# Performance work log

Hardware: AMD Instinct MI355X
Metric: run time of the kernel (lower is better)

Reference implementation:

```python
import jax, jax.numpy as jnp
import numpy as np

B, T, I, L, D, O = 256, 512, 512, 128, 4, 2
LN_EPS = 1e-5

def setup_inputs() -> dict:
    key = jax.random.key(0)
    ks = jax.random.split(key, 7)
    x = jax.random.normal(ks[0], (B, T, I), jnp.float32)
    # Xavier-ish scaling keeps the recurrence numerically tame
    W_in = jax.random.normal(ks[1], (L, D, I), jnp.float32) * (1.0 / np.sqrt(I))
    W_liquid = jax.random.normal(ks[2], (L, D, L), jnp.float32) * (1.0 / np.sqrt(L))
    W_gate = jax.random.normal(ks[3], (L, D), jnp.float32)
    b_liquid = jnp.zeros((L,), jnp.float32)
    W_out = jax.random.normal(ks[4], (O, L), jnp.float32) * (1.0 / np.sqrt(L))
    b_out = jnp.zeros((O,), jnp.float32)
    ln_w = jnp.ones((L,), jnp.float32)
    ln_b = jnp.zeros((L,), jnp.float32)
    leaky_rate = jnp.asarray(0.3, jnp.float32)
    return {"x": x, "W_in": W_in, "W_liquid": W_liquid, "W_gate": W_gate,
            "b_liquid": b_liquid, "W_out": W_out, "b_out": b_out,
            "ln_w": ln_w, "ln_b": ln_b, "leaky_rate": leaky_rate}

def reference(x, W_in, W_liquid, W_gate, b_liquid, W_out, b_out, ln_w, ln_b, leaky_rate):
    # Liquid dendritic RNN. Dropout is identity (eval mode).
    gate = jax.nn.sigmoid(W_gate)                                   # [L,D]
    # Input branch has no recurrent dependency -> batch it over all timesteps
    in_br = jax.nn.relu(jnp.einsum('ldi,bti->btld', W_in, x))       # [B,T,L,D]
    merged_in = jnp.einsum('btld,ld->btl', in_br, gate)             # [B,T,L]
    alpha = jax.nn.sigmoid(leaky_rate)

    def step(state, m_in_t):                                        # state [B,L]
        rec_br = jax.nn.relu(jnp.einsum('ldh,bh->bld', W_liquid, state))
        merged_rec = jnp.einsum('bld,ld->bl', rec_br, gate)
        li = m_in_t + merged_rec + b_liquid                         # [B,L]
        mu = jnp.mean(li, axis=-1, keepdims=True)
        var = jnp.var(li, axis=-1, keepdims=True)
        li = (li - mu) * jax.lax.rsqrt(var + LN_EPS) * ln_w + ln_b
        new_state = (1.0 - alpha) * state + alpha * jnp.tanh(li)
        return new_state, None

    state0 = jnp.zeros((x.shape[0], W_in.shape[0]), x.dtype)
    final_state, _ = jax.lax.scan(step, state0, jnp.swapaxes(merged_in, 0, 1))
    return final_state @ W_out.T + b_out                            # [B,O]
```

## Files before the change

### kernel.cpp

```cpp
#include <hip/hip_runtime.h>
#include <hip/hip_bf16.h>
#include <stdint.h>


typedef __bf16 bf16x8 __attribute__((ext_vector_type(8)));
typedef float f32x4_t __attribute__((ext_vector_type(4)));

__device__ inline unsigned short f2bf(float f) {
    union { float f; unsigned u; } v; v.f = f;
    unsigned r = v.u + 0x7fffu + ((v.u >> 16) & 1u);
    return (unsigned short)(r >> 16);
}

__device__ inline unsigned cvt_pk_bf16(float lo, float hi) {
    unsigned r;
    asm("v_cvt_pk_bf16_f32 %0, %1, %2" : "=v"(r) : "v"(lo), "v"(hi));
    return r;
}

__device__ inline void lds_barrier() {
    asm volatile("s_waitcnt lgkmcnt(0)" ::: "memory");
    __builtin_amdgcn_s_barrier();
}

__device__ inline float bfly16_add(float x) {
    float a, b;
    asm volatile("v_mov_b32 %0, %2\n\t"
                 "v_mov_b32 %1, %2\n\t"
                 "v_permlane16_swap_b32 %0, %1"
                 : "=&v"(a), "=&v"(b) : "v"(x));
    return a + b;
}
__device__ inline float bfly32_add(float x) {
    float a, b;
    asm volatile("v_mov_b32 %0, %2\n\t"
                 "v_mov_b32 %1, %2\n\t"
                 "v_permlane32_swap_b32 %0, %1"
                 : "=&v"(a), "=&v"(b) : "v"(x));
    return a + b;
}

__global__ __launch_bounds__(256, 2)
void gemm_in_kernel(const float* __restrict__ x, const float* __restrict__ W_in,
                    const float* __restrict__ W_gate, const float* __restrict__ b_liq,
                    float* __restrict__ mt)
{
    __shared__ unsigned short As[128 * 32];
    __shared__ unsigned short Bs[128 * 32];

    const int tid = threadIdx.x;
    const int wid  = blockIdx.x;
    const int xcd  = wid & 7;
    const int slot = wid >> 3;
    const int n0 = (slot & 3) * 128;
    const int m0 = ((slot >> 2) + xcd * 128) * 128;

    const int lane = tid & 63;
    const int widw = tid >> 6;
    const int wr = widw >> 1, wc = widw & 1;
    const int fr = lane & 15, fq = lane >> 4;

    f32x4_t acc[4][4];
    #pragma unroll
    for (int i = 0; i < 4; ++i)
        #pragma unroll
        for (int j = 0; j < 4; ++j)
            acc[i][j] = (f32x4_t){0.f, 0.f, 0.f, 0.f};

    for (int k0 = 0; k0 < 512; k0 += 32) {
        #pragma unroll
        for (int p = 0; p < 4; ++p) {
            int ch = tid + p * 256;
            int r  = ch >> 3;
            int c  = ch & 7;
            float4 va = *(const float4*)(x    + (size_t)(m0 + r) * 512 + k0 + c * 4);
            float4 vb = *(const float4*)(W_in + (size_t)(n0 + r) * 512 + k0 + c * 4);
            uint2 ua, ub;
            ua.x = cvt_pk_bf16(va.x, va.y);
            ua.y = cvt_pk_bf16(va.z, va.w);
            ub.x = cvt_pk_bf16(vb.x, vb.y);
            ub.y = cvt_pk_bf16(vb.z, vb.w);
            *(uint2*)(&As[r * 32 + c * 4]) = ua;
            *(uint2*)(&Bs[r * 32 + c * 4]) = ub;
        }
        __syncthreads();

        bf16x8 af[4], bfr[4];
        #pragma unroll
        for (int mi = 0; mi < 4; ++mi)
            af[mi] = *(const bf16x8*)(&As[(wr * 64 + mi * 16 + fr) * 32 + fq * 8]);
        #pragma unroll
        for (int ni = 0; ni < 4; ++ni)
            bfr[ni] = *(const bf16x8*)(&Bs[(wc * 64 + ni * 16 + fr) * 32 + fq * 8]);

        #pragma unroll
        for (int mi = 0; mi < 4; ++mi)
            #pragma unroll
            for (int ni = 0; ni < 4; ++ni)
                acc[mi][ni] = __builtin_amdgcn_mfma_f32_16x16x32_bf16(
                                  af[mi], bfr[ni], acc[mi][ni], 0, 0, 0);
        __syncthreads();
    }

    float gv[4], blq[4];
    #pragma unroll
    for (int ni = 0; ni < 4; ++ni) {
        int n = n0 + wc * 64 + ni * 16 + fr;
        gv[ni]  = 1.f / (1.f + __expf(-W_gate[n]));
        blq[ni] = b_liq[n >> 2];
    }
    #pragma unroll
    for (int mi = 0; mi < 4; ++mi) {
        #pragma unroll
        for (int ni = 0; ni < 4; ++ni) {
            int n = n0 + wc * 64 + ni * 16 + fr;
            int l = n >> 2;
            #pragma unroll
            for (int j = 0; j < 4; ++j) {
                float v = acc[mi][ni][j];
                float r = fmaxf(v, 0.f) * gv[ni];
                r += __shfl_xor(r, 1);
                r += __shfl_xor(r, 2);
                if ((lane & 3) == 0) {
                    int row = m0 + wr * 64 + mi * 16 + fq * 4 + j;
                    int bb = row >> 9;
                    int tt = row & 511;
                    mt[(size_t)bb * 65536 + (size_t)l * 512 + tt] = r + blq[ni];
                }
            }
        }
    }
}

__global__ __launch_bounds__(256, 1)
void scan_kernel(const float* __restrict__ mt, const float* __restrict__ W_liq,
                 const float* __restrict__ W_gate, const float* __restrict__ W_out,
                 const float* __restrict__ b_out, const float* __restrict__ ln_w,
                 const float* __restrict__ ln_b, const float* __restrict__ leaky,
                 float* __restrict__ out)
{
    __shared__ __align__(16) unsigned short s_bf[128];
    __shared__ __align__(16) float red2[8];
    __shared__ float s_final[128];

    const int tid  = threadIdx.x;
    const int b    = blockIdx.x;
    const int lane = tid & 63;
    const int w    = tid >> 6;
    const int fr   = lane & 15;
    const int fq   = lane >> 4;

    bf16x8 wfrag[8][4];
    #pragma unroll
    for (int mi = 0; mi < 8; ++mi) {
        const int n = w * 128 + mi * 16 + fr;
        const float gn = 1.f / (1.f + __expf(-W_gate[n]));
        const float* wrow = W_liq + (size_t)n * 128;
        #pragma unroll
        for (int kk = 0; kk < 4; ++kk) {
            float4 f0 = *(const float4*)(wrow + kk * 32 + fq * 8);
            float4 f1 = *(const float4*)(wrow + kk * 32 + fq * 8 + 4);
            union { unsigned short u[8]; bf16x8 v; } cv;
            cv.u[0] = f2bf(gn * f0.x); cv.u[1] = f2bf(gn * f0.y);
            cv.u[2] = f2bf(gn * f0.z); cv.u[3] = f2bf(gn * f0.w);
            cv.u[4] = f2bf(gn * f1.x); cv.u[5] = f2bf(gn * f1.y);
            cv.u[6] = f2bf(gn * f1.z); cv.u[7] = f2bf(gn * f1.w);
            wfrag[mi][kk] = cv.v;
        }
    }

    size_t midx[8];
    #pragma unroll
    for (int mi = 0; mi < 8; ++mi)
        midx[mi] = (size_t)b * 65536 + (size_t)(w * 32 + mi * 4 + fq) * 512;

    const int l_own  = w * 32 + (fr & 7) * 4 + fq;
    const float K2   = 2.8853900817779268f;
    const float lw2  = ln_w[l_own] * K2;
    const float lb2  = ln_b[l_own] * K2;
    const float alpha = 1.f / (1.f + __expf(-leaky[0]));
    const float oma   = 1.f - alpha;
    const float n2a   = -2.f * alpha;

    float s_own = 0.f;
    float c0    = alpha;

    float4 cur4[8], nxt4[8];
    #pragma unroll
    for (int mi = 0; mi < 8; ++mi) cur4[mi] = *(const float4*)(mt + midx[mi]);
    #pragma unroll
    for (int mi = 0; mi < 8; ++mi) nxt4[mi] = *(const float4*)(mt + midx[mi] + 4);

    if (tid < 64) ((unsigned*)s_bf)[tid] = 0u;
    lds_barrier();

    const f32x4_t z = {0.f, 0.f, 0.f, 0.f};

    for (int ts = 0; ts < 512; ts += 4) {
        float4 ld4[8];
        if (ts < 504) {
            #pragma unroll
            for (int mi = 0; mi < 8; ++mi)
                ld4[mi] = *(const float4*)(mt + midx[mi] + ts + 8);
        }

        #pragma unroll
        for (int ph = 0; ph < 4; ++ph) {
            bf16x8 bfr[4];
            #pragma unroll
            for (int kk = 0; kk < 4; ++kk)
                bfr[kk] = *(const bf16x8*)(&s_bf[kk * 32 + fq * 8]);

            f32x4_t a0[8], a1[8];
            #pragma unroll
            for (int mi = 0; mi < 8; ++mi) {
                a0[mi] = __builtin_amdgcn_mfma_f32_16x16x32_bf16(wfrag[mi][0], bfr[0], z, 0, 0, 0);
                a1[mi] = __builtin_amdgcn_mfma_f32_16x16x32_bf16(wfrag[mi][2], bfr[2], z, 0, 0, 0);
            }
            #pragma unroll
            for (int mi = 0; mi < 8; ++mi) {
                a0[mi] = __builtin_amdgcn_mfma_f32_16x16x32_bf16(wfrag[mi][1], bfr[1], a0[mi], 0, 0, 0);
                a1[mi] = __builtin_amdgcn_mfma_f32_16x16x32_bf16(wfrag[mi][3], bfr[3], a1[mi], 0, 0, 0);
            }

            float li[8];
            float v1a = 0.f, v1b = 0.f, v2a = 0.f, v2b = 0.f;
            #pragma unroll
            for (int mi = 0; mi < 8; ++mi) {
                f32x4_t s4 = a0[mi] + a1[mi];
                float mr = (fmaxf(s4[0], 0.f) + fmaxf(s4[1], 0.f))
                         + (fmaxf(s4[2], 0.f) + fmaxf(s4[3], 0.f));
                li[mi] = cur4[mi][ph] + mr;
                if (mi & 1) { v1b += li[mi]; v2b = fmaf(li[mi], li[mi], v2b); }
                else        { v1a += li[mi]; v2a = fmaf(li[mi], li[mi], v2a); }
            }
            float v1 = v1a + v1b, v2 = v2a + v2b;

            float sa = (fr & 1) ? li[1] : li[0];
            float sb = (fr & 1) ? li[3] : li[2];
            float sc = (fr & 1) ? li[5] : li[4];
            float sd = (fr & 1) ? li[7] : li[6];
            float se = (fr & 2) ? sb : sa;
            float sf = (fr & 2) ? sd : sc;
            float li_o = (fr & 4) ? sf : se;

            v1 = bfly16_add(v1);  v2 = bfly16_add(v2);
            v1 = bfly32_add(v1);  v2 = bfly32_add(v2);
            if (lane == 0) { red2[2 * w] = v1; red2[2 * w + 1] = v2; }
            lds_barrier();

            float4 r0 = *(const float4*)&red2[0], r1 = *(const float4*)&red2[4];
            float S1 = (r0.x + r0.z) + (r1.x + r1.z);
            float S2 = (r0.y + r0.w) + (r1.y + r1.w);
            float mean = S1 * (1.f / 128.f);
            float var  = fmaf(-mean, mean, S2 * (1.f / 128.f));
            float rstd = __builtin_amdgcn_rsqf(var + 1e-5f);

            float q  = rstd * lw2;
            float xn = fmaf(li_o, q, fmaf(-mean, q, lb2));
            float e  = __builtin_amdgcn_exp2f(xn);
            float r  = __builtin_amdgcn_rcpf(e + 1.f);
            s_own    = fmaf(n2a, r, c0);
            c0       = fmaf(oma, s_own, alpha);

            unsigned cvt;
            asm("v_cvt_pk_bf16_f32 %0, %1, %2" : "=v"(cvt) : "v"(s_own), "v"(0.f));
            if (fr < 8) s_bf[l_own] = (unsigned short)cvt;
            lds_barrier();
        }

        #pragma unroll
        for (int mi = 0; mi < 8; ++mi) cur4[mi] = nxt4[mi];
        if (ts < 504) {
            #pragma unroll
            for (int mi = 0; mi < 8; ++mi) nxt4[mi] = ld4[mi];
        }
    }

    if (fr < 8) s_final[l_own] = s_own;
    __syncthreads();
    if (tid < 2) {
        float accO = b_out[tid];
        #pragma unroll
        for (int h = 0; h < 128; ++h)
            accO = fmaf(s_final[h], W_out[tid * 128 + h], accO);
        out[b * 2 + tid] = accO;
    }
}

extern "C" void kernel_launch(void* const* d_in, const int* in_sizes, int n_in,
                              void* d_out, int out_size, void* d_ws, size_t ws_size,
                              hipStream_t stream)
{
    const float* x      = (const float*)d_in[0];
    const float* W_in   = (const float*)d_in[1];
    const float* W_liq  = (const float*)d_in[2];
    const float* W_gate = (const float*)d_in[3];
    const float* b_liq  = (const float*)d_in[4];
    const float* W_out  = (const float*)d_in[5];
    const float* b_out  = (const float*)d_in[6];
    const float* ln_w   = (const float*)d_in[7];
    const float* ln_b   = (const float*)d_in[8];
    const float* leaky  = (const float*)d_in[9];
    float* out = (float*)d_out;
    float* mt  = (float*)d_ws;

    gemm_in_kernel<<<4096, 256, 0, stream>>>(x, W_in, W_gate, b_liq, mt);
    scan_kernel<<<256, 256, 0, stream>>>(mt, W_liq, W_gate,
                                         W_out, b_out, ln_w, ln_b, leaky, out);
}
```

Before: 630.4 us.

## Overlap input GEMM with recurrent scan via chunked fused kernel and flags

Splits the input-projection GEMM into time chunks: chunk 0 runs first, then a fused kernel launches the 256 scan blocks first and the remaining GEMM tiles behind them. Each GEMM tile increments a per-(batch, chunk) atomic flag, and scan blocks spin on that flag before prefetching the next chunk's inputs. The goal is to hide most of the GEMM time behind the latency-bound scan. The trade-offs are spin-wait overhead and a memset. Correctness relies on the scan blocks being scheduled before the GEMM blocks and on having enough workspace; otherwise the code falls back to the two-kernel path.

```diff
diff --git a/kernel.cpp b/kernel.cpp
--- a/kernel.cpp
+++ b/kernel.cpp
@@ -40,21 +40,14 @@
     return a + b;
 }
 
-__global__ __launch_bounds__(256, 2)
-void gemm_in_kernel(const float* __restrict__ x, const float* __restrict__ W_in,
-                    const float* __restrict__ W_gate, const float* __restrict__ b_liq,
-                    float* __restrict__ mt)
-{
-    __shared__ unsigned short As[128 * 32];
-    __shared__ unsigned short Bs[128 * 32];
-
-    const int tid = threadIdx.x;
-    const int wid  = blockIdx.x;
-    const int xcd  = wid & 7;
-    const int slot = wid >> 3;
-    const int n0 = (slot & 3) * 128;
-    const int m0 = ((slot >> 2) + xcd * 128) * 128;
-
+__device__ __forceinline__ void gemm_tile(const float* __restrict__ x,
+                                          const float* __restrict__ W_in,
+                                          const float* __restrict__ W_gate,
+                                          const float* __restrict__ b_liq,
+                                          float* __restrict__ mt,
+                                          unsigned short* As, unsigned short* Bs,
+                                          int m0, int n0, int tid)
+{
     const int lane = tid & 63;
     const int widw = tid >> 6;
     const int wr = widw >> 1, wc = widw & 1;
@@ -132,19 +125,49 @@
     }
 }
 
-__global__ __launch_bounds__(256, 1)
-void scan_kernel(const float* __restrict__ mt, const float* __restrict__ W_liq,
+__global__ __launch_bounds__(256, 2)
+void gemm_all_kernel(const float* __restrict__ x, const float* __restrict__ W_in,
+                     const float* __restrict__ W_gate, const float* __restrict__ b_liq,
+                     float* __restrict__ mt)
+{
+    __shared__ unsigned short As[128 * 32];
+    __shared__ unsigned short Bs[128 * 32];
+    const int wid  = blockIdx.x;
+    const int xcd  = wid & 7;
+    const int slot = wid >> 3;
+    const int n0 = (slot & 3) * 128;
+    const int m0 = ((slot >> 2) + xcd * 128) * 128;
+    gemm_tile(x, W_in, W_gate, b_liq, mt, As, Bs, m0, n0, threadIdx.x);
+}
+
+__global__ __launch_bounds__(256, 2)
+void gemm_chunk0_kernel(const float* __restrict__ x, const float* __restrict__ W_in,
+                        const float* __restrict__ W_gate, const float* __restrict__ b_liq,
+                        float* __restrict__ mt)
+{
+    __shared__ unsigned short As[128 * 32];
+    __shared__ unsigned short Bs[128 * 32];
+    const int wid  = blockIdx.x;
+    const int xcd  = wid & 7;
+    const int slot = wid >> 3;
+    const int n0 = (slot & 3) * 128;
+    const int b2 = xcd * 32 + (slot >> 2);
+    const int m0 = b2 * 512;
+    gemm_tile(x, W_in, W_gate, b_liq, mt, As, Bs, m0, n0, threadIdx.x);
+}
+
+__device__ __forceinline__ void scan_body(int b,
+                 const float* __restrict__ mt, const float* __restrict__ W_liq,
                  const float* __restrict__ W_gate, const float* __restrict__ W_out,
                  const float* __restrict__ b_out, const float* __restrict__ ln_w,
                  const float* __restrict__ ln_b, const float* __restrict__ leaky,
-                 float* __restrict__ out)
+                 float* __restrict__ out, const int* flags)
 {
     __shared__ __align__(16) unsigned short s_bf[128];
     __shared__ __align__(16) float red2[8];
     __shared__ float s_final[128];
 
     const int tid  = threadIdx.x;
-    const int b    = blockIdx.x;
     const int lane = tid & 63;
     const int w    = tid >> 6;
     const int fr   = lane & 15;
@@ -197,6 +220,18 @@
     const f32x4_t z = {0.f, 0.f, 0.f, 0.f};
 
     for (int ts = 0; ts < 512; ts += 4) {
+        if (flags && (ts & 127) == 120 && ts < 500) {
+            if (tid == 0) {
+                const int idx = b * 4 + ((ts + 8) >> 7);
+                while (__hip_atomic_load(&flags[idx], __ATOMIC_RELAXED,
+                                         __HIP_MEMORY_SCOPE_AGENT) < 4)
+                    __builtin_amdgcn_s_sleep(32);
+                (void)__hip_atomic_load(&flags[idx], __ATOMIC_ACQUIRE,
+                                        __HIP_MEMORY_SCOPE_AGENT);
+            }
+            __syncthreads();
+        }
+
         float4 ld4[8];
         if (ts < 504) {
             #pragma unroll
@@ -286,6 +321,49 @@
             accO = fmaf(s_final[h], W_out[tid * 128 + h], accO);
         out[b * 2 + tid] = accO;
     }
+}
+
+__global__ __launch_bounds__(256, 1)
+void scan_kernel(const float* __restrict__ mt, const float* __restrict__ W_liq,
+                 const float* __restrict__ W_gate, const float* __restrict__ W_out,
+                 const float* __restrict__ b_out, const float* __restrict__ ln_w,
+                 const float* __restrict__ ln_b, const float* __restrict__ leaky,
+                 float* __restrict__ out)
+{
+    scan_body(blockIdx.x, mt, W_liq, W_gate, W_out, b_out, ln_w, ln_b, leaky,
+              out, nullptr);
+}
+
+__global__ __launch_bounds__(256, 2)
+void fused_kernel(const float* __restrict__ x, const float* __restrict__ W_in,
+                  const float* __restrict__ W_liq, const float* __restrict__ W_gate,
+                  const float* __restrict__ b_liq, const float* __restrict__ W_out,
+                  const float* __restrict__ b_out, const float* __restrict__ ln_w,
+                  const float* __restrict__ ln_b, const float* __restrict__ leaky,
+                  float* __restrict__ mt, float* __restrict__ out,
+                  int* __restrict__ flags)
+{
+    if (blockIdx.x >= 256) {
+        __shared__ unsigned short As[128 * 32];
+        __shared__ unsigned short Bs[128 * 32];
+        const int id2  = blockIdx.x - 256;
+        const int cc   = 1 + (id2 >> 10);
+        const int w2   = id2 & 1023;
+        const int xcd  = w2 & 7;
+        const int slot = w2 >> 3;
+        const int n0 = (slot & 3) * 128;
+        const int b2 = xcd * 32 + (slot >> 2);
+        const int m0 = b2 * 512 + cc * 128;
+        gemm_tile(x, W_in, W_gate, b_liq, mt, As, Bs, m0, n0, threadIdx.x);
+        __syncthreads();
+        if (threadIdx.x == 0) {
+            __threadfence();
+            atomicAdd(&flags[b2 * 4 + cc], 1);
+        }
+        return;
+    }
+    scan_body(blockIdx.x, mt, W_liq, W_gate, W_out, b_out, ln_w, ln_b, leaky,
+              out, flags);
 }
 
 extern "C" void kernel_launch(void* const* d_in, const int* in_sizes, int n_in,
@@ -304,8 +382,18 @@
     const float* leaky  = (const float*)d_in[9];
     float* out = (float*)d_out;
     float* mt  = (float*)d_ws;
-
-    gemm_in_kernel<<<4096, 256, 0, stream>>>(x, W_in, W_gate, b_liq, mt);
-    scan_kernel<<<256, 256, 0, stream>>>(mt, W_liq, W_gate,
-                                         W_out, b_out, ln_w, ln_b, leaky, out);
-}
+    const size_t MT_BYTES = 256ull * 512 * 128 * sizeof(float);
+
+    if (ws_size >= MT_BYTES + 4096) {
+        int* flags = (int*)((char*)d_ws + MT_BYTES);
+        hipMemsetAsync(flags, 0, 4096, stream);
+        gemm_chunk0_kernel<<<1024, 256, 0, stream>>>(x, W_in, W_gate, b_liq, mt);
+        fused_kernel<<<3328, 256, 0, stream>>>(x, W_in, W_liq, W_gate, b_liq,
+                                               W_out, b_out, ln_w, ln_b, leaky,
+                                               mt, out, flags);
+    } else {
+        gemm_all_kernel<<<4096, 256, 0, stream>>>(x, W_in, W_gate, b_liq, mt);
+        scan_kernel<<<256, 256, 0, stream>>>(mt, W_liq, W_gate, W_out, b_out,
+                                             ln_w, ln_b, leaky, out);
+    }
+}
```

After: 879.5 us. 1.4x slower.
